# Kernel optimization log

Measured on AMD Instinct MI355X. Metric: run time of the kernel, lower is better.

Reference implementation:

```python
import jax, jax.numpy as jnp
import numpy as np

B, S, E = 2, 2049, 512
H, WIN = 8, 1024
D = E // H


def setup_inputs() -> dict:
    key = jax.random.key(0)
    ks = jax.random.split(key, 11)
    sc = 0.02
    return {
        "x": jax.random.normal(ks[0], (B, S, E), dtype=jnp.float32),
        "Wq": jax.random.normal(ks[1], (E, E), dtype=jnp.float32) * sc,
        "bq": jnp.zeros((E,), dtype=jnp.float32),
        "Wk": jax.random.normal(ks[2], (E, E), dtype=jnp.float32) * sc,
        "bk": jnp.zeros((E,), dtype=jnp.float32),
        "Wv": jax.random.normal(ks[3], (E, E), dtype=jnp.float32) * sc,
        "bv": jnp.zeros((E,), dtype=jnp.float32),
        "Wo": jax.random.normal(ks[4], (E, E), dtype=jnp.float32) * sc,
        "bo": jnp.zeros((E,), dtype=jnp.float32),
        "w_gate": jax.random.normal(ks[5], (2 * E,), dtype=jnp.float32) * sc,
        "b_gate": jnp.zeros((), dtype=jnp.float32),
    }


def reference(x, Wq, bq, Wk, bk, Wv, bv, Wo, bo, w_gate, b_gate):
    scale = D ** -0.5
    q_flat = x @ Wq + bq  # [B,S,E]
    k_flat = x @ Wk + bk
    v_flat = x @ Wv + bv
    q = q_flat.reshape(B, S, H, D).transpose(0, 2, 1, 3)  # [B,H,S,D]
    k = k_flat.reshape(B, S, H, D).transpose(0, 2, 1, 3)
    v = v_flat.reshape(B, S, H, D).transpose(0, 2, 1, 3)

    scores = jnp.einsum("bhqd,bhkd->bhqk", q, k) * scale  # [B,H,S,S]

    # Gaussian positional bias: -0.5*|i-j|^2/sigma^2, sigma = window/2
    pos = jnp.arange(S)
    dist = jnp.abs(pos[:, None] - pos[None, :]).astype(jnp.float32)
    sigma = WIN / 2.0
    bias = -0.5 * dist ** 2 / (sigma ** 2)  # [S,S]
    scores = scores + bias[None, None]

    # Pairwise gate: sigmoid(concat(q_i,k_j) @ w + b) == sigmoid(q_i.wq + k_j.wk + b)
    gq = q_flat @ w_gate[:E]       # [B,S]
    gk = k_flat @ w_gate[E:]       # [B,S]
    gates = jax.nn.sigmoid(gq[:, :, None] + gk[:, None, :] + b_gate)  # [B,S,S]
    scores = scores * gates[:, None]  # broadcast over heads

    local_mask = jnp.where(dist <= WIN, 0.0, -jnp.inf).astype(jnp.float32)
    scores = scores + local_mask[None, None]

    attn = jax.nn.softmax(scores, axis=-1)
    out = jnp.einsum("bhqk,bhkd->bhqd", attn, v)  # [B,H,S,D]
    out = out.transpose(0, 2, 1, 3).reshape(B, S, E)
    return out @ Wo + bo
```

## Files before the change

### kernel.cpp

```cpp
#include <hip/hip_runtime.h>
#include <cstdint>
#include <cstddef>

#define B_ 2
#define S_ 2049
#define E_ 512
#define H_ 8
#define WIN_ 1024
#define MROWS (B_*S_)
#define SP_ 2176
#define GBUFN 4104
#define BHS_ (B_*H_*S_)

typedef unsigned short ushort_t;
typedef __attribute__((ext_vector_type(8))) short bf16x8;
typedef __attribute__((ext_vector_type(4))) float f32x4;

#define MFMA16(a,b,c) __builtin_amdgcn_mfma_f32_16x16x32_bf16(a,b,c,0,0,0)

__device__ __forceinline__ ushort_t f2bf(float f) {
  unsigned int u = __float_as_uint(f);
  u += 0x7fffu + ((u >> 16) & 1u);
  return (ushort_t)(u >> 16);
}
__device__ __forceinline__ float bf2f(ushort_t h) {
  return __uint_as_float(((unsigned int)h) << 16);
}

__global__ __launch_bounds__(256) void convert_w_kernel(
    const float* __restrict__ W0, const float* __restrict__ W1,
    const float* __restrict__ W2, const float* __restrict__ W3,
    ushort_t* __restrict__ Wt_all, ushort_t* __restrict__ WoHi,
    float* __restrict__ gacc)
{
  __shared__ float tile[32][33];
  int z = blockIdx.z;
  if (z == 3) {
    int gz = (blockIdx.x * 16 + blockIdx.y) * 256 + threadIdx.x;
    if (gz < 2 * GBUFN) gacc[gz] = 0.f;
  }
  const float* W = (z == 0) ? W0 : (z == 1) ? W1 : (z == 2) ? W2 : W3;
  int k0 = blockIdx.x * 32, n0 = blockIdx.y * 32;
  int r = threadIdx.x >> 5, c = threadIdx.x & 31;
#pragma unroll
  for (int i = 0; i < 4; ++i) {
    int rr = r + i * 8;
    tile[rr][c] = W[(size_t)(k0 + rr) * E_ + n0 + c];
  }
  __syncthreads();
#pragma unroll
  for (int i = 0; i < 4; ++i) {
    int rr = r + i * 8;
    float v = tile[c][rr];
    size_t dst = (size_t)(n0 + rr) * E_ + k0 + c;
    if (z < 3) Wt_all[(size_t)z * E_ * E_ + dst] = f2bf(v);
    else       WoHi[dst] = f2bf(v);
  }
}

__global__ __launch_bounds__(256) void gemm_qkv_kernel(
    const float* __restrict__ x, const ushort_t* __restrict__ Wt_all,
    const float* __restrict__ bq, const float* __restrict__ bk,
    const float* __restrict__ bv, const float* __restrict__ wg,
    ushort_t* __restrict__ qkb, ushort_t* __restrict__ vT,
    float* __restrict__ gacc)
{
  __shared__ __align__(16) ushort_t As[64][40];
  __shared__ __align__(16) ushort_t Bs[128][40];
  int tid = threadIdx.x;
  int lane = tid & 63, w = tid >> 6;
  int l15 = lane & 15, quad = lane >> 4;
  int wm = (w & 1) * 32, wn = (w >> 1) * 64;
  int z = blockIdx.z;
  const ushort_t* Wt = Wt_all + (size_t)z * E_ * E_;
  const float* bias = (z == 0) ? bq : (z == 1) ? bk : bv;
  int bt = blockIdx.x;
  int bg2 = bt / 33;
  int bm = (bt - bg2 * 33) * 64;
  int bn = blockIdx.y * 128;
  size_t rowbase = (size_t)bg2 * S_;

  int ar = tid >> 2, acq = (tid & 3) * 8;
  int ai = bm + ar; if (ai >= S_) ai = S_ - 1;
  const float* ap = x + (rowbase + ai) * E_ + acq;
  int br = tid >> 1, bcq = (tid & 1) * 16;
  const ushort_t* bp = Wt + (size_t)(bn + br) * E_ + bcq;

  const f32x4 fz = {0.f, 0.f, 0.f, 0.f};
  f32x4 acc[2][4];
#pragma unroll
  for (int mt = 0; mt < 2; ++mt)
#pragma unroll
    for (int nt = 0; nt < 4; ++nt) acc[mt][nt] = fz;

  float4 pa0 = *(const float4*)ap, pa1 = *(const float4*)(ap + 4);
  int4  pb0 = *(const int4*)bp,   pb1 = *(const int4*)(bp + 8);

  for (int k0 = 0; k0 < E_; k0 += 32) {
    __syncthreads();
    int kn = (k0 + 32 < E_) ? (k0 + 32) : k0;
    float4 na0 = *(const float4*)(ap + kn), na1 = *(const float4*)(ap + kn + 4);
    int4  nb0 = *(const int4*)(bp + kn),   nb1 = *(const int4*)(bp + kn + 8);
    union { int4 v; ushort_t u[8]; } cv;
    cv.u[0] = f2bf(pa0.x); cv.u[1] = f2bf(pa0.y); cv.u[2] = f2bf(pa0.z); cv.u[3] = f2bf(pa0.w);
    cv.u[4] = f2bf(pa1.x); cv.u[5] = f2bf(pa1.y); cv.u[6] = f2bf(pa1.z); cv.u[7] = f2bf(pa1.w);
    *(int4*)&As[ar][acq] = cv.v;
    *(int4*)&Bs[br][bcq] = pb0; *(int4*)&Bs[br][bcq + 8] = pb1;
    __syncthreads();
    bf16x8 a[2], bfr[4];
#pragma unroll
    for (int mt = 0; mt < 2; ++mt) a[mt] = *(const bf16x8*)&As[wm + mt * 16 + l15][quad * 8];
#pragma unroll
    for (int nt = 0; nt < 4; ++nt) bfr[nt] = *(const bf16x8*)&Bs[wn + nt * 16 + l15][quad * 8];
#pragma unroll
    for (int mt = 0; mt < 2; ++mt)
#pragma unroll
      for (int nt = 0; nt < 4; ++nt)
        acc[mt][nt] = MFMA16(a[mt], bfr[nt], acc[mt][nt]);
    pa0 = na0; pa1 = na1; pb0 = nb0; pb1 = nb1;
  }

  float bb[4];
#pragma unroll
  for (int nt = 0; nt < 4; ++nt) bb[nt] = bias[bn + wn + nt * 16 + l15];

  if (z < 2) {
    ushort_t* C = qkb + (size_t)z * MROWS * E_;
#pragma unroll
    for (int mt = 0; mt < 2; ++mt)
#pragma unroll
      for (int nt = 0; nt < 4; ++nt)
#pragma unroll
        for (int r = 0; r < 4; ++r) {
          int i = bm + wm + mt * 16 + quad * 4 + r;
          if (i < S_)
            C[(rowbase + i) * E_ + bn + wn + nt * 16 + l15] = f2bf(acc[mt][nt][r] + bb[nt]);
        }
    const float* wgp = wg + (size_t)z * E_;
    float wv[4];
#pragma unroll
    for (int nt = 0; nt < 4; ++nt) wv[nt] = wgp[bn + wn + nt * 16 + l15];
    float* gp = gacc + (size_t)z * GBUFN;
#pragma unroll
    for (int mt = 0; mt < 2; ++mt)
#pragma unroll
      for (int r = 0; r < 4; ++r) {
        float s = 0.f;
#pragma unroll
        for (int nt = 0; nt < 4; ++nt) s = fmaf(acc[mt][nt][r] + bb[nt], wv[nt], s);
        s += __shfl_xor(s, 1, 16); s += __shfl_xor(s, 2, 16);
        s += __shfl_xor(s, 4, 16); s += __shfl_xor(s, 8, 16);
        int i = bm + wm + mt * 16 + quad * 4 + r;
        if (l15 == 0 && i < S_) atomicAdd(&gp[rowbase + i], s);
      }
  } else {
    ushort_t* lt = &Bs[0][0];
    int ti = tid >> 2, tc = (tid & 3) * 16;
#pragma unroll
    for (int hh = 0; hh < 2; ++hh) {
      __syncthreads();
      if ((w >> 1) == hh) {
#pragma unroll
        for (int mt = 0; mt < 2; ++mt)
#pragma unroll
          for (int nt = 0; nt < 4; ++nt) {
            int d = nt * 16 + l15;
#pragma unroll
            for (int r = 0; r < 4; ++r) {
              int il = wm + mt * 16 + quad * 4 + r;
              lt[d * 72 + il] = f2bf(acc[mt][nt][r] + bb[nt]);
            }
          }
      }
      __syncthreads();
      int hg = (bn >> 6) + hh;
      union { int4 q[2]; ushort_t u[16]; } tv;
      tv.q[0] = *(const int4*)&lt[ti * 72 + tc];
      tv.q[1] = *(const int4*)&lt[ti * 72 + tc + 8];
      size_t vrow = ((size_t)(bg2 * H_ + hg) * 64 + ti) * SP_;
#pragma unroll
      for (int c8 = 0; c8 < 2; ++c8) {
        int i2 = bm + tc + c8 * 8;
        if (i2 + 7 < S_) {
          *(int4*)&vT[vrow + i2] = tv.q[c8];
        } else {
#pragma unroll
          for (int e = 0; e < 8; ++e)
            if (i2 + e < S_) vT[vrow + i2 + e] = tv.u[c8 * 8 + e];
        }
      }
    }
  }
}

__global__ __launch_bounds__(256) void attn_kernel(
    const ushort_t* __restrict__ qb, const ushort_t* __restrict__ kb,
    const ushort_t* __restrict__ vT, const float* __restrict__ gq_raw,
    const float* __restrict__ gk_raw, const float* __restrict__ bgate,
    float* __restrict__ Opart, float* __restrict__ Lpart)
{
  __shared__ __align__(16) ushort_t Ks[64][72];
  __shared__ __align__(16) ushort_t Vt[64][72];
  __shared__ __align__(16) ushort_t Ps[4][16][72];
  __shared__ float gbs[704];

  int tid = threadIdx.x;
  int lane = tid & 63, w = tid >> 6;
  int l15 = lane & 15, quad = lane >> 4;

  int sub = blockIdx.x % 48;
  int qidx = blockIdx.x / 48;
  int off = (qidx + 1) >> 1;
  int qt = 16 + ((qidx & 1) ? -off : off);
  int bh = sub & 15, third = sub >> 4;
  int h = bh & 7, b = bh >> 3;
  int i0 = qt * 64;
  const float coef = -0.5f / (512.f * 512.f);

  int i = i0 + w * 16 + l15;
  int ic = (i < S_) ? i : S_ - 1;
  bf16x8 qf0 = *(const bf16x8*)&qb[((size_t)(b * S_ + ic)) * E_ + h * 64 + quad * 8];
  bf16x8 qf1 = *(const bf16x8*)&qb[((size_t)(b * S_ + ic)) * E_ + h * 64 + 32 + quad * 8];
#pragma unroll
  for (int e = 0; e < 8; ++e) {
    qf0[e] = (short)f2bf(bf2f((ushort_t)qf0[e]) * 0.125f);
    qf1[e] = (short)f2bf(bf2f((ushort_t)qf1[e]) * 0.125f);
  }
  float av = __expf(-(gq_raw[b * S_ + ic] + bgate[0]));
  float fdi = (i < S_) ? (float)i : -1e5f;

  int jlo = i0 - WIN_; if (jlo < 0) jlo = 0;
  int jt_lo = jlo >> 6;
  int jhi = i0 + 63 + WIN_; if (jhi > S_ - 1) jhi = S_ - 1;
  int jt_hi = jhi >> 6;
  int L = jt_hi - jt_lo + 1;
  int n0 = (L + 2) / 3, n1 = (L + 1) / 3;
  int myLo = jt_lo + ((third == 0) ? 0 : (third == 1) ? n0 : n0 + n1);
  int cnt = (third == 0) ? n0 : (third == 1) ? n1 : L - n0 - n1;
  int myHi = myLo + cnt - 1;
  int jbase = myLo << 6;
  int nwin = cnt << 6;

  for (int tt = tid; tt < nwin; tt += 256) {
    int j = jbase + tt; int jc = (j < S_) ? j : S_ - 1;
    gbs[tt] = __expf(-gk_raw[b * S_ + jc]);
  }

  int srow = tid >> 2, scol = (tid & 3) * 16;
  const ushort_t* kb_base = kb + (size_t)b * S_ * E_ + h * 64 + scol;
  const ushort_t* vb_base = vT + ((size_t)(b * H_ + h) * 64 + srow) * SP_ + scol;

  int4 ka0, ka1, va0, va1;
  {
    int jc0 = jbase + srow; if (jc0 > S_ - 1) jc0 = S_ - 1;
    const int4* kp = (const int4*)(kb_base + (size_t)jc0 * E_);
    ka0 = kp[0]; ka1 = kp[1];
    const int4* vp = (const int4*)(vb_base + jbase);
    va0 = vp[0]; va1 = vp[1];
  }

  const f32x4 fz = {0.f, 0.f, 0.f, 0.f};
  f32x4 Ov[4] = {fz, fz, fz, fz};
  float l_run = 0.f;

  for (int jt = myLo; jt <= myHi; ++jt) {
    int j0 = jt << 6;
    __syncthreads();
    int jn = (jt < myHi) ? ((jt + 1) << 6) : j0;
    int jcn = jn + srow; if (jcn > S_ - 1) jcn = S_ - 1;
    const int4* kp = (const int4*)(kb_base + (size_t)jcn * E_);
    int4 nk0 = kp[0], nk1 = kp[1];
    const int4* vp = (const int4*)(vb_base + jn);
    int4 nv0 = vp[0], nv1 = vp[1];
    *(int4*)&Ks[srow][scol] = ka0; *(int4*)&Ks[srow][scol + 8] = ka1;
    *(int4*)&Vt[srow][scol] = va0; *(int4*)&Vt[srow][scol + 8] = va1;
    __syncthreads();

    f32x4 st[4];
#pragma unroll
    for (int nt = 0; nt < 4; ++nt) {
      bf16x8 kf0 = *(const bf16x8*)&Ks[nt * 16 + l15][quad * 8];
      bf16x8 kf1 = *(const bf16x8*)&Ks[nt * 16 + l15][32 + quad * 8];
      f32x4 s = MFMA16(kf0, qf0, fz);
      st[nt] = MFMA16(kf1, qf1, s);
    }

    bool full = ((j0 + 63 - i0) <= WIN_) && ((i0 + 63 - j0) <= WIN_)
                && (j0 + 63 < S_) && (i0 + 63 < S_);
    float ps = 0.f;
    float jq = (float)(j0 + quad * 4);
    if (full) {
#pragma unroll
      for (int nt = 0; nt < 4; ++nt) {
        f32x4 g4 = *(const f32x4*)&gbs[(j0 - jbase) + nt * 16 + quad * 4];
#pragma unroll
        for (int r = 0; r < 4; ++r) {
          float f = fdi - (jq + (float)(nt * 16 + r));
          float gate = __builtin_amdgcn_rcpf(fmaf(av, g4[r], 1.f));
          float p = __expf(fmaf(f * f, coef, st[nt][r]) * gate);
          st[nt][r] = p; ps += p;
        }
      }
    } else {
#pragma unroll
      for (int nt = 0; nt < 4; ++nt) {
        f32x4 g4 = *(const f32x4*)&gbs[(j0 - jbase) + nt * 16 + quad * 4];
#pragma unroll
        for (int r = 0; r < 4; ++r) {
          int j = j0 + nt * 16 + quad * 4 + r;
          float fj = (j < S_) ? (float)j : 1e5f;
          float f = fdi - fj;
          float gate = __builtin_amdgcn_rcpf(fmaf(av, g4[r], 1.f));
          float t = fmaf(f * f, coef, st[nt][r]) * gate;
          t = (__builtin_fabsf(f) <= 1024.f) ? t : -1e30f;
          float p = __expf(t);
          st[nt][r] = p; ps += p;
        }
      }
    }
    ps += __shfl_xor(ps, 16);
    ps += __shfl_xor(ps, 32);
    l_run += ps;

#pragma unroll
    for (int nt = 0; nt < 4; ++nt) {
      uint2 pk;
      pk.x = (unsigned int)f2bf(st[nt][0]) | ((unsigned int)f2bf(st[nt][1]) << 16);
      pk.y = (unsigned int)f2bf(st[nt][2]) | ((unsigned int)f2bf(st[nt][3]) << 16);
      *(uint2*)&Ps[w][l15][nt * 16 + quad * 4] = pk;
    }
    bf16x8 p0 = *(const bf16x8*)&Ps[w][l15][quad * 8];
    bf16x8 p1 = *(const bf16x8*)&Ps[w][l15][32 + quad * 8];
#pragma unroll
    for (int nt = 0; nt < 4; ++nt) {
      bf16x8 v0 = *(const bf16x8*)&Vt[nt * 16 + l15][quad * 8];
      bf16x8 v1 = *(const bf16x8*)&Vt[nt * 16 + l15][32 + quad * 8];
      Ov[nt] = MFMA16(p0, v0, Ov[nt]);
      Ov[nt] = MFMA16(p1, v1, Ov[nt]);
    }
    ka0 = nk0; ka1 = nk1; va0 = nv0; va1 = nv1;
  }

  if (lane < 16) {
    int irow = i0 + w * 16 + lane;
    if (irow < S_)
      Lpart[(size_t)third * BHS_ + (size_t)(b * H_ + h) * S_ + irow] = l_run;
  }
#pragma unroll
  for (int r = 0; r < 4; ++r) {
    int irow = i0 + w * 16 + quad * 4 + r;
    if (irow < S_) {
      size_t base = ((size_t)third * BHS_ + (size_t)(b * H_ + h) * S_ + irow) * 64;
#pragma unroll
      for (int nt = 0; nt < 4; ++nt)
        Opart[base + nt * 16 + l15] = Ov[nt][r];
    }
  }
}

__global__ __launch_bounds__(256) void combine_kernel(
    const float* __restrict__ Opart, const float* __restrict__ Lpart,
    ushort_t* __restrict__ ahi, ushort_t* __restrict__ alo)
{
  int tid = threadIdx.x;
  int gi = blockIdx.x * 16 + (tid >> 4);
  int d4 = tid & 15;
  int b = gi / (H_ * S_);
  int rem = gi - b * (H_ * S_);
  int h = rem / S_;
  int i = rem - h * S_;
  size_t p0 = (size_t)(b * H_ + h) * S_ + i;
  float l = Lpart[p0] + Lpart[p0 + (size_t)BHS_] + Lpart[p0 + 2 * (size_t)BHS_];
  float inv = 1.f / l;
  const float* op = Opart + p0 * 64 + d4 * 4;
  float4 o1 = *(const float4*)op;
  float4 o2 = *(const float4*)(op + (size_t)BHS_ * 64);
  float4 o3 = *(const float4*)(op + 2 * (size_t)BHS_ * 64);
  float o[4] = {(o1.x + o2.x + o3.x) * inv, (o1.y + o2.y + o3.y) * inv,
                (o1.z + o2.z + o3.z) * inv, (o1.w + o2.w + o3.w) * inv};
  ushort4 hi, lo;
  hi.x = f2bf(o[0]); lo.x = f2bf(o[0] - bf2f(hi.x));
  hi.y = f2bf(o[1]); lo.y = f2bf(o[1] - bf2f(hi.y));
  hi.z = f2bf(o[2]); lo.z = f2bf(o[2] - bf2f(hi.z));
  hi.w = f2bf(o[3]); lo.w = f2bf(o[3] - bf2f(hi.w));
  size_t oidx = ((size_t)b * S_ + i) * E_ + h * 64 + d4 * 4;
  *(ushort4*)&ahi[oidx] = hi;
  *(ushort4*)&alo[oidx] = lo;
}

__global__ __launch_bounds__(256) void gemm_out_kernel(
    const ushort_t* __restrict__ Ahi, const ushort_t* __restrict__ Alo,
    const ushort_t* __restrict__ Whi, const float* __restrict__ bias,
    float* __restrict__ C)
{
  __shared__ __align__(16) ushort_t AsH[64][40];
  __shared__ __align__(16) ushort_t AsL[64][40];
  __shared__ __align__(16) ushort_t BsW[64][40];
  int tid = threadIdx.x;
  int lane = tid & 63, w = tid >> 6;
  int l15 = lane & 15, quad = lane >> 4;
  int bm = blockIdx.x * 64, bn = blockIdx.y * 64;
  int sr = tid >> 2, sc = (tid & 3) * 8;
  int am = bm + sr; if (am >= MROWS) am = MROWS - 1;
  const ushort_t* ahp = Ahi + (size_t)am * E_ + sc;
  const ushort_t* alp = Alo + (size_t)am * E_ + sc;
  const ushort_t* bp  = Whi + (size_t)(bn + sr) * E_ + sc;

  const f32x4 fz = {0.f, 0.f, 0.f, 0.f};
  f32x4 acc[4] = {fz, fz, fz, fz};

  int4 ph = *(const int4*)ahp, pl = *(const int4*)alp, pb = *(const int4*)bp;

  for (int k0 = 0; k0 < E_; k0 += 32) {
    __syncthreads();
    int kn = (k0 + 32 < E_) ? (k0 + 32) : k0;
    int4 nh = *(const int4*)(ahp + kn);
    int4 nl = *(const int4*)(alp + kn);
    int4 nb = *(const int4*)(bp + kn);
    *(int4*)&AsH[sr][sc] = ph;
    *(int4*)&AsL[sr][sc] = pl;
    *(int4*)&BsW[sr][sc] = pb;
    __syncthreads();
    bf16x8 ah = *(const bf16x8*)&AsH[w * 16 + l15][quad * 8];
    bf16x8 al = *(const bf16x8*)&AsL[w * 16 + l15][quad * 8];
#pragma unroll
    for (int nt = 0; nt < 4; ++nt) {
      bf16x8 bw = *(const bf16x8*)&BsW[nt * 16 + l15][quad * 8];
      acc[nt] = MFMA16(ah, bw, acc[nt]);
      acc[nt] = MFMA16(al, bw, acc[nt]);
    }
    ph = nh; pl = nl; pb = nb;
  }
#pragma unroll
  for (int nt = 0; nt < 4; ++nt) {
    float bb = bias[bn + nt * 16 + l15];
#pragma unroll
    for (int r = 0; r < 4; ++r) {
      int m = bm + w * 16 + quad * 4 + r;
      if (m < MROWS)
        C[(size_t)m * E_ + bn + nt * 16 + l15] = acc[nt][r] + bb;
    }
  }
}

extern "C" void kernel_launch(void* const* d_in, const int* in_sizes, int n_in,
                              void* d_out, int out_size, void* d_ws, size_t ws_size,
                              hipStream_t stream) {
  const float* x  = (const float*)d_in[0];
  const float* Wq = (const float*)d_in[1];
  const float* bq = (const float*)d_in[2];
  const float* Wk = (const float*)d_in[3];
  const float* bk = (const float*)d_in[4];
  const float* Wv = (const float*)d_in[5];
  const float* bv = (const float*)d_in[6];
  const float* Wo = (const float*)d_in[7];
  const float* bo = (const float*)d_in[8];
  const float* wg = (const float*)d_in[9];
  const float* bg = (const float*)d_in[10];

  char* p = (char*)d_ws;
  ushort_t* Wt_all = (ushort_t*)p; p += (size_t)3 * E_ * E_ * 2;
  ushort_t* WoHi   = (ushort_t*)p; p += (size_t)E_ * E_ * 2;
  ushort_t* qkb    = (ushort_t*)p; p += (size_t)2 * MROWS * E_ * 2;
  ushort_t* vT     = (ushort_t*)p; p += (size_t)B_ * H_ * 64 * SP_ * 2;
  float*    gacc   = (float*)p;    p += (size_t)2 * GBUFN * 4;
  float*    Opart  = (float*)p;    p += (size_t)3 * BHS_ * 64 * 4;
  float*    Lpart  = (float*)p;    p += (size_t)3 * BHS_ * 4;
  ushort_t* aHi    = qkb;
  ushort_t* aLo    = qkb + (size_t)MROWS * E_;

  hipLaunchKernelGGL(convert_w_kernel, dim3(16, 16, 4), dim3(256), 0, stream,
                     Wq, Wk, Wv, Wo, Wt_all, WoHi, gacc);
  hipLaunchKernelGGL(gemm_qkv_kernel, dim3(66, 4, 3), dim3(256), 0, stream,
                     x, Wt_all, bq, bk, bv, wg, qkb, vT, gacc);
  hipLaunchKernelGGL(attn_kernel, dim3(33 * 48), dim3(256), 0, stream,
                     qkb, qkb + (size_t)MROWS * E_, vT, gacc, gacc + GBUFN, bg,
                     Opart, Lpart);
  hipLaunchKernelGGL(combine_kernel, dim3(2049), dim3(256), 0, stream,
                     Opart, Lpart, aHi, aLo);
  hipLaunchKernelGGL(gemm_out_kernel, dim3(65, 8), dim3(256), 0, stream,
                     aHi, aLo, WoHi, bo, (float*)d_out);
}
```

Measured before the change: 170.0 us.

## Load V directly to registers, use exp2, enlarge GEMM tiles

The QKV projection GEMM now stages a 64-wide k slice per iteration, halving its barrier count. The output GEMM uses 64x128 tiles with 2x4 MFMA subtiles per wave to improve operand reuse. In the attention kernel, V fragments are read directly from global memory into registers instead of being staged through shared memory, and exp is replaced by exp2 with log2e folded into the query scale and bias coefficient. The tradeoffs are more register pressure and more LDS footprint in the GEMMs, and V global loads that are no longer shared across waves.

Measured after the change: 248.0 us. +45.9%, slower.

```diff
diff --git a/kernel.cpp b/kernel.cpp
--- a/kernel.cpp
+++ b/kernel.cpp
@@ -65,8 +65,8 @@
     ushort_t* __restrict__ qkb, ushort_t* __restrict__ vT,
     float* __restrict__ gacc)
 {
-  __shared__ __align__(16) ushort_t As[64][40];
-  __shared__ __align__(16) ushort_t Bs[128][40];
+  __shared__ __align__(16) ushort_t As[64][72];
+  __shared__ __align__(16) ushort_t Bs[128][72];
   int tid = threadIdx.x;
   int lane = tid & 63, w = tid >> 6;
   int l15 = lane & 15, quad = lane >> 4;
@@ -80,10 +80,10 @@
   int bn = blockIdx.y * 128;
   size_t rowbase = (size_t)bg2 * S_;
 
-  int ar = tid >> 2, acq = (tid & 3) * 8;
+  int ar = tid >> 2, acq = (tid & 3) * 16;
   int ai = bm + ar; if (ai >= S_) ai = S_ - 1;
   const float* ap = x + (rowbase + ai) * E_ + acq;
-  int br = tid >> 1, bcq = (tid & 1) * 16;
+  int br = tid >> 1, bcq = (tid & 1) * 32;
   const ushort_t* bp = Wt + (size_t)(bn + br) * E_ + bcq;
 
   const f32x4 fz = {0.f, 0.f, 0.f, 0.f};
@@ -93,31 +93,41 @@
 #pragma unroll
     for (int nt = 0; nt < 4; ++nt) acc[mt][nt] = fz;
 
-  float4 pa0 = *(const float4*)ap, pa1 = *(const float4*)(ap + 4);
-  int4  pb0 = *(const int4*)bp,   pb1 = *(const int4*)(bp + 8);
-
-  for (int k0 = 0; k0 < E_; k0 += 32) {
+  float4 pa[4]; int4 pb[4];
+#pragma unroll
+  for (int t = 0; t < 4; ++t) { pa[t] = *(const float4*)(ap + t * 4); pb[t] = *(const int4*)(bp + t * 8); }
+
+  for (int k0 = 0; k0 < E_; k0 += 64) {
     __syncthreads();
-    int kn = (k0 + 32 < E_) ? (k0 + 32) : k0;
-    float4 na0 = *(const float4*)(ap + kn), na1 = *(const float4*)(ap + kn + 4);
-    int4  nb0 = *(const int4*)(bp + kn),   nb1 = *(const int4*)(bp + kn + 8);
-    union { int4 v; ushort_t u[8]; } cv;
-    cv.u[0] = f2bf(pa0.x); cv.u[1] = f2bf(pa0.y); cv.u[2] = f2bf(pa0.z); cv.u[3] = f2bf(pa0.w);
-    cv.u[4] = f2bf(pa1.x); cv.u[5] = f2bf(pa1.y); cv.u[6] = f2bf(pa1.z); cv.u[7] = f2bf(pa1.w);
-    *(int4*)&As[ar][acq] = cv.v;
-    *(int4*)&Bs[br][bcq] = pb0; *(int4*)&Bs[br][bcq + 8] = pb1;
+    int kn = (k0 + 64 < E_) ? (k0 + 64) : k0;
+    float4 na[4]; int4 nb[4];
+#pragma unroll
+    for (int t = 0; t < 4; ++t) { na[t] = *(const float4*)(ap + kn + t * 4); nb[t] = *(const int4*)(bp + kn + t * 8); }
+    union { int4 v[2]; ushort_t u[16]; } cv;
+#pragma unroll
+    for (int t = 0; t < 4; ++t) {
+      cv.u[t*4+0] = f2bf(pa[t].x); cv.u[t*4+1] = f2bf(pa[t].y);
+      cv.u[t*4+2] = f2bf(pa[t].z); cv.u[t*4+3] = f2bf(pa[t].w);
+    }
+    *(int4*)&As[ar][acq] = cv.v[0]; *(int4*)&As[ar][acq + 8] = cv.v[1];
+#pragma unroll
+    for (int t = 0; t < 4; ++t) *(int4*)&Bs[br][bcq + t * 8] = pb[t];
     __syncthreads();
-    bf16x8 a[2], bfr[4];
-#pragma unroll
-    for (int mt = 0; mt < 2; ++mt) a[mt] = *(const bf16x8*)&As[wm + mt * 16 + l15][quad * 8];
-#pragma unroll
-    for (int nt = 0; nt < 4; ++nt) bfr[nt] = *(const bf16x8*)&Bs[wn + nt * 16 + l15][quad * 8];
-#pragma unroll
-    for (int mt = 0; mt < 2; ++mt)
-#pragma unroll
-      for (int nt = 0; nt < 4; ++nt)
-        acc[mt][nt] = MFMA16(a[mt], bfr[nt], acc[mt][nt]);
-    pa0 = na0; pa1 = na1; pb0 = nb0; pb1 = nb1;
+#pragma unroll
+    for (int half = 0; half < 2; ++half) {
+      bf16x8 a[2], bfr[4];
+#pragma unroll
+      for (int mt = 0; mt < 2; ++mt) a[mt] = *(const bf16x8*)&As[wm + mt * 16 + l15][half * 32 + quad * 8];
+#pragma unroll
+      for (int nt = 0; nt < 4; ++nt) bfr[nt] = *(const bf16x8*)&Bs[wn + nt * 16 + l15][half * 32 + quad * 8];
+#pragma unroll
+      for (int mt = 0; mt < 2; ++mt)
+#pragma unroll
+        for (int nt = 0; nt < 4; ++nt)
+          acc[mt][nt] = MFMA16(a[mt], bfr[nt], acc[mt][nt]);
+    }
+#pragma unroll
+    for (int t = 0; t < 4; ++t) { pa[t] = na[t]; pb[t] = nb[t]; }
   }
 
   float bb[4];
@@ -200,7 +210,6 @@
     float* __restrict__ Opart, float* __restrict__ Lpart)
 {
   __shared__ __align__(16) ushort_t Ks[64][72];
-  __shared__ __align__(16) ushort_t Vt[64][72];
   __shared__ __align__(16) ushort_t Ps[4][16][72];
   __shared__ float gbs[704];
 
@@ -215,7 +224,9 @@
   int bh = sub & 15, third = sub >> 4;
   int h = bh & 7, b = bh >> 3;
   int i0 = qt * 64;
-  const float coef = -0.5f / (512.f * 512.f);
+  const float LOG2E = 1.44269504f;
+  const float coef2 = (-0.5f / (512.f * 512.f)) * LOG2E;
+  const float QSC = 0.125f * LOG2E;
 
   int i = i0 + w * 16 + l15;
   int ic = (i < S_) ? i : S_ - 1;
@@ -223,8 +234,8 @@
   bf16x8 qf1 = *(const bf16x8*)&qb[((size_t)(b * S_ + ic)) * E_ + h * 64 + 32 + quad * 8];
 #pragma unroll
   for (int e = 0; e < 8; ++e) {
-    qf0[e] = (short)f2bf(bf2f((ushort_t)qf0[e]) * 0.125f);
-    qf1[e] = (short)f2bf(bf2f((ushort_t)qf1[e]) * 0.125f);
+    qf0[e] = (short)f2bf(bf2f((ushort_t)qf0[e]) * QSC);
+    qf1[e] = (short)f2bf(bf2f((ushort_t)qf1[e]) * QSC);
   }
   float av = __expf(-(gq_raw[b * S_ + ic] + bgate[0]));
   float fdi = (i < S_) ? (float)i : -1e5f;
@@ -248,15 +259,16 @@
 
   int srow = tid >> 2, scol = (tid & 3) * 16;
   const ushort_t* kb_base = kb + (size_t)b * S_ * E_ + h * 64 + scol;
-  const ushort_t* vb_base = vT + ((size_t)(b * H_ + h) * 64 + srow) * SP_ + scol;
-
-  int4 ka0, ka1, va0, va1;
+  const ushort_t* vrow[4];
+#pragma unroll
+  for (int nt = 0; nt < 4; ++nt)
+    vrow[nt] = vT + ((size_t)(b * H_ + h) * 64 + nt * 16 + l15) * SP_ + quad * 8;
+
+  int4 ka0, ka1;
   {
     int jc0 = jbase + srow; if (jc0 > S_ - 1) jc0 = S_ - 1;
     const int4* kp = (const int4*)(kb_base + (size_t)jc0 * E_);
     ka0 = kp[0]; ka1 = kp[1];
-    const int4* vp = (const int4*)(vb_base + jbase);
-    va0 = vp[0]; va1 = vp[1];
   }
 
   const f32x4 fz = {0.f, 0.f, 0.f, 0.f};
@@ -270,11 +282,15 @@
     int jcn = jn + srow; if (jcn > S_ - 1) jcn = S_ - 1;
     const int4* kp = (const int4*)(kb_base + (size_t)jcn * E_);
     int4 nk0 = kp[0], nk1 = kp[1];
-    const int4* vp = (const int4*)(vb_base + jn);
-    int4 nv0 = vp[0], nv1 = vp[1];
     *(int4*)&Ks[srow][scol] = ka0; *(int4*)&Ks[srow][scol + 8] = ka1;
-    *(int4*)&Vt[srow][scol] = va0; *(int4*)&Vt[srow][scol + 8] = va1;
     __syncthreads();
+
+    bf16x8 vf0[4], vf1[4];
+#pragma unroll
+    for (int nt = 0; nt < 4; ++nt) {
+      vf0[nt] = *(const bf16x8*)(vrow[nt] + j0);
+      vf1[nt] = *(const bf16x8*)(vrow[nt] + j0 + 32);
+    }
 
     f32x4 st[4];
 #pragma unroll
@@ -288,16 +304,16 @@
     bool full = ((j0 + 63 - i0) <= WIN_) && ((i0 + 63 - j0) <= WIN_)
                 && (j0 + 63 < S_) && (i0 + 63 < S_);
     float ps = 0.f;
-    float jq = (float)(j0 + quad * 4);
+    float fq = fdi - (float)(j0 + quad * 4);
     if (full) {
 #pragma unroll
       for (int nt = 0; nt < 4; ++nt) {
         f32x4 g4 = *(const f32x4*)&gbs[(j0 - jbase) + nt * 16 + quad * 4];
 #pragma unroll
         for (int r = 0; r < 4; ++r) {
-          float f = fdi - (jq + (float)(nt * 16 + r));
+          float f = fq - (float)(nt * 16 + r);
           float gate = __builtin_amdgcn_rcpf(fmaf(av, g4[r], 1.f));
-          float p = __expf(fmaf(f * f, coef, st[nt][r]) * gate);
+          float p = __builtin_amdgcn_exp2f(fmaf(f * f, coef2, st[nt][r]) * gate);
           st[nt][r] = p; ps += p;
         }
       }
@@ -311,9 +327,9 @@
           float fj = (j < S_) ? (float)j : 1e5f;
           float f = fdi - fj;
           float gate = __builtin_amdgcn_rcpf(fmaf(av, g4[r], 1.f));
-          float t = fmaf(f * f, coef, st[nt][r]) * gate;
+          float t = fmaf(f * f, coef2, st[nt][r]) * gate;
           t = (__builtin_fabsf(f) <= 1024.f) ? t : -1e30f;
-          float p = __expf(t);
+          float p = __builtin_amdgcn_exp2f(t);
           st[nt][r] = p; ps += p;
         }
       }
@@ -333,12 +349,10 @@
     bf16x8 p1 = *(const bf16x8*)&Ps[w][l15][32 + quad * 8];
 #pragma unroll
     for (int nt = 0; nt < 4; ++nt) {
-      bf16x8 v0 = *(const bf16x8*)&Vt[nt * 16 + l15][quad * 8];
-      bf16x8 v1 = *(const bf16x8*)&Vt[nt * 16 + l15][32 + quad * 8];
-      Ov[nt] = MFMA16(p0, v0, Ov[nt]);
-      Ov[nt] = MFMA16(p1, v1, Ov[nt]);
-    }
-    ka0 = nk0; ka1 = nk1; va0 = nv0; va1 = nv1;
+      Ov[nt] = MFMA16(p0, vf0[nt], Ov[nt]);
+      Ov[nt] = MFMA16(p1, vf1[nt], Ov[nt]);
+    }
+    ka0 = nk0; ka1 = nk1;
   }
 
   if (lane < 16) {
@@ -395,51 +409,68 @@
 {
   __shared__ __align__(16) ushort_t AsH[64][40];
   __shared__ __align__(16) ushort_t AsL[64][40];
-  __shared__ __align__(16) ushort_t BsW[64][40];
+  __shared__ __align__(16) ushort_t BsW[128][40];
   int tid = threadIdx.x;
   int lane = tid & 63, w = tid >> 6;
   int l15 = lane & 15, quad = lane >> 4;
-  int bm = blockIdx.x * 64, bn = blockIdx.y * 64;
+  int wm = (w & 1) * 32, wn = (w >> 1) * 64;
+  int bm = blockIdx.x * 64, bn = blockIdx.y * 128;
+
   int sr = tid >> 2, sc = (tid & 3) * 8;
   int am = bm + sr; if (am >= MROWS) am = MROWS - 1;
   const ushort_t* ahp = Ahi + (size_t)am * E_ + sc;
   const ushort_t* alp = Alo + (size_t)am * E_ + sc;
-  const ushort_t* bp  = Whi + (size_t)(bn + sr) * E_ + sc;
+  int br = tid >> 1, bc = (tid & 1) * 16;
+  const ushort_t* bp = Whi + (size_t)(bn + br) * E_ + bc;
 
   const f32x4 fz = {0.f, 0.f, 0.f, 0.f};
-  f32x4 acc[4] = {fz, fz, fz, fz};
-
-  int4 ph = *(const int4*)ahp, pl = *(const int4*)alp, pb = *(const int4*)bp;
+  f32x4 acc[2][4];
+#pragma unroll
+  for (int mt = 0; mt < 2; ++mt)
+#pragma unroll
+    for (int nt = 0; nt < 4; ++nt) acc[mt][nt] = fz;
+
+  int4 ph = *(const int4*)ahp, pl = *(const int4*)alp;
+  int4 pb0 = *(const int4*)bp, pb1 = *(const int4*)(bp + 8);
 
   for (int k0 = 0; k0 < E_; k0 += 32) {
     __syncthreads();
     int kn = (k0 + 32 < E_) ? (k0 + 32) : k0;
     int4 nh = *(const int4*)(ahp + kn);
     int4 nl = *(const int4*)(alp + kn);
-    int4 nb = *(const int4*)(bp + kn);
+    int4 nb0 = *(const int4*)(bp + kn), nb1 = *(const int4*)(bp + kn + 8);
     *(int4*)&AsH[sr][sc] = ph;
     *(int4*)&AsL[sr][sc] = pl;
-    *(int4*)&BsW[sr][sc] = pb;
+    *(int4*)&BsW[br][bc] = pb0; *(int4*)&BsW[br][bc + 8] = pb1;
     __syncthreads();
-    bf16x8 ah = *(const bf16x8*)&AsH[w * 16 + l15][quad * 8];
-    bf16x8 al = *(const bf16x8*)&AsL[w * 16 + l15][quad * 8];
-#pragma unroll
-    for (int nt = 0; nt < 4; ++nt) {
-      bf16x8 bw = *(const bf16x8*)&BsW[nt * 16 + l15][quad * 8];
-      acc[nt] = MFMA16(ah, bw, acc[nt]);
-      acc[nt] = MFMA16(al, bw, acc[nt]);
-    }
-    ph = nh; pl = nl; pb = nb;
+    bf16x8 ah[2], al[2], bw[4];
+#pragma unroll
+    for (int mt = 0; mt < 2; ++mt) {
+      ah[mt] = *(const bf16x8*)&AsH[wm + mt * 16 + l15][quad * 8];
+      al[mt] = *(const bf16x8*)&AsL[wm + mt * 16 + l15][quad * 8];
+    }
+#pragma unroll
+    for (int nt = 0; nt < 4; ++nt) bw[nt] = *(const bf16x8*)&BsW[wn + nt * 16 + l15][quad * 8];
+#pragma unroll
+    for (int mt = 0; mt < 2; ++mt)
+#pragma unroll
+      for (int nt = 0; nt < 4; ++nt) {
+        acc[mt][nt] = MFMA16(ah[mt], bw[nt], acc[mt][nt]);
+        acc[mt][nt] = MFMA16(al[mt], bw[nt], acc[mt][nt]);
+      }
+    ph = nh; pl = nl; pb0 = nb0; pb1 = nb1;
   }
 #pragma unroll
   for (int nt = 0; nt < 4; ++nt) {
-    float bb = bias[bn + nt * 16 + l15];
-#pragma unroll
-    for (int r = 0; r < 4; ++r) {
-      int m = bm + w * 16 + quad * 4 + r;
-      if (m < MROWS)
-        C[(size_t)m * E_ + bn + nt * 16 + l15] = acc[nt][r] + bb;
-    }
+    float bb = bias[bn + wn + nt * 16 + l15];
+#pragma unroll
+    for (int mt = 0; mt < 2; ++mt)
+#pragma unroll
+      for (int r = 0; r < 4; ++r) {
+        int m = bm + wm + mt * 16 + quad * 4 + r;
+        if (m < MROWS)
+          C[(size_t)m * E_ + bn + wn + nt * 16 + l15] = acc[mt][nt][r] + bb;
+      }
   }
 }
 
@@ -478,6 +509,6 @@
                      Opart, Lpart);
   hipLaunchKernelGGL(combine_kernel, dim3(2049), dim3(256), 0, stream,
                      Opart, Lpart, aHi, aLo);
-  hipLaunchKernelGGL(gemm_out_kernel, dim3(65, 8), dim3(256), 0, stream,
+  hipLaunchKernelGGL(gemm_out_kernel, dim3(65, 4), dim3(256), 0, stream,
                      aHi, aLo, WoHi, bo, (float*)d_out);
 }
```
